# Kernel optimization log

Hardware: AMD Instinct MI355X
Metric: run time of the kernel (lower is better)

The kernel has to match this reference:

```python
import jax, jax.numpy as jnp
import numpy as np

N = 20000          # nodes
E = 320000         # edges
H = 128            # hidden_channels
A = 512            # aerial feature dim
SPOT = 20000
DIST_UNIT = 50
NEMB = SPOT // DIST_UNIT
RATIO = 0.25       # neighbor_ratio


def setup_inputs() -> dict:
    key = jax.random.key(0)
    ks = jax.random.split(key, 12)
    x = jax.random.normal(ks[0], (N, H), jnp.float32)
    edge_index = jax.random.randint(ks[1], (2, E), 0, N)
    distances = jax.random.randint(ks[2], (E,), 0, SPOT)
    aerial_emb = jax.random.normal(ks[3], (N, A), jnp.float32)
    s = lambda k, shape, fan: jax.random.normal(k, shape, jnp.float32) / np.sqrt(fan).astype(np.float32)
    W_lin = s(ks[4], (H, H), H)
    b_lin = jnp.zeros((H,), jnp.float32)
    W_q = s(ks[5], (H + A + H, H), H + A + H)
    b_q = jnp.zeros((H,), jnp.float32)
    W_v = s(ks[6], (H, H), H)
    b_v = jnp.zeros((H,), jnp.float32)
    dist_table = jax.random.normal(ks[7], (NEMB, H), jnp.float32)  # init.normal_ like torch
    W_l = s(ks[8], (H, H), H)   # SAGE lin_l (neighbor aggr), with bias
    b_l = jnp.zeros((H,), jnp.float32)
    W_r = s(ks[9], (H, H), H)   # SAGE lin_r (root), no bias in PyG default
    return dict(x=x, edge_index=edge_index, distances=distances, aerial_emb=aerial_emb,
                W_lin=W_lin, b_lin=b_lin, W_q=W_q, b_q=b_q, W_v=W_v, b_v=b_v,
                dist_table=dist_table, W_l=W_l, b_l=b_l, W_r=W_r)


def reference(x, edge_index, distances, aerial_emb, W_lin, b_lin, W_q, b_q, W_v, b_v, dist_table, W_l, b_l, W_r):
    n = x.shape[0]
    e = edge_index.shape[1]
    k = int(e * RATIO)  # static: number of sampled edges

    x = x @ W_lin + b_lin                                  # [N, H]
    src, tgt = edge_index[0], edge_index[1]
    source_x = x[src]                                      # [E, H]
    target_x = x[tgt]                                      # [E, H]
    source_aerial = aerial_emb[src]                        # [E, A]
    dist_x = dist_table[distances // DIST_UNIT]            # [E, H]

    query = jnp.concatenate([source_x, source_aerial, dist_x], axis=1) @ W_q + b_q  # [E, H]
    value = target_x @ W_v + b_v                           # [E, H]
    logits = -jnp.linalg.norm(query - value, axis=1)       # [E]
    logprob = jax.nn.log_softmax(logits, axis=0)

    # torch.multinomial(prob, k) without replacement == Gumbel top-k on log-probs
    u = jax.random.uniform(jax.random.key(42), (e,), jnp.float32)
    gumbel = -jnp.log(-jnp.log(u + 1e-20) + 1e-20)
    _, sel = jax.lax.top_k(logprob + gumbel, k)            # [k] selected edge ids
    src_s = src[sel]
    tgt_s = tgt[sel]

    # SAGEConv (mean aggregation): out = lin_l(mean_j x_j) + lin_r(x)
    msg = jax.ops.segment_sum(x[src_s], tgt_s, num_segments=n)              # [N, H]
    deg = jax.ops.segment_sum(jnp.ones((k,), x.dtype), tgt_s, num_segments=n)
    aggr = msg / jnp.maximum(deg, 1.0)[:, None]
    out = aggr @ W_l + b_l + x @ W_r                       # [N, H]
    return out
```

## Files before the change

### kernel.cpp

```cpp
#include <hip/hip_runtime.h>
#include <stdint.h>

#define N_NODES 20000
#define E_EDGES 320000
#define H_DIM 128
#define A_DIM 512
#define NEMB_N 400
#define K_SEL 80000u
#define NB1 16384
#define NB2 16384
#define CAND_MAX 8192
#define LO_F (-128.0f)
#define SCALE1 (16384.0f / 160.0f)

struct SelState {
    int b1; unsigned cum1; unsigned r1;
    int b2; unsigned cum2; unsigned r2;
    unsigned long long T;
};

__device__ __forceinline__ uint32_t rotl32(uint32_t x, int r) {
    return (x << r) | (x >> (32 - r));
}

__device__ __forceinline__ void threefry2x32(uint32_t k0, uint32_t k1,
                                             uint32_t& x0, uint32_t& x1) {
    uint32_t ks0 = k0, ks1 = k1, ks2 = k0 ^ k1 ^ 0x1BD11BDAu;
    x0 += ks0; x1 += ks1;
    x0 += x1; x1 = rotl32(x1, 13); x1 ^= x0;
    x0 += x1; x1 = rotl32(x1, 15); x1 ^= x0;
    x0 += x1; x1 = rotl32(x1, 26); x1 ^= x0;
    x0 += x1; x1 = rotl32(x1, 6);  x1 ^= x0;
    x0 += ks1; x1 += ks2 + 1u;
    x0 += x1; x1 = rotl32(x1, 17); x1 ^= x0;
    x0 += x1; x1 = rotl32(x1, 29); x1 ^= x0;
    x0 += x1; x1 = rotl32(x1, 16); x1 ^= x0;
    x0 += x1; x1 = rotl32(x1, 24); x1 ^= x0;
    x0 += ks2; x1 += ks0 + 2u;
    x0 += x1; x1 = rotl32(x1, 13); x1 ^= x0;
    x0 += x1; x1 = rotl32(x1, 15); x1 ^= x0;
    x0 += x1; x1 = rotl32(x1, 26); x1 ^= x0;
    x0 += x1; x1 = rotl32(x1, 6);  x1 ^= x0;
    x0 += ks0; x1 += ks1 + 3u;
    x0 += x1; x1 = rotl32(x1, 17); x1 ^= x0;
    x0 += x1; x1 = rotl32(x1, 29); x1 ^= x0;
    x0 += x1; x1 = rotl32(x1, 16); x1 ^= x0;
    x0 += x1; x1 = rotl32(x1, 24); x1 ^= x0;
    x0 += ks1; x1 += ks2 + 4u;
    x0 += x1; x1 = rotl32(x1, 13); x1 ^= x0;
    x0 += x1; x1 = rotl32(x1, 15); x1 ^= x0;
    x0 += x1; x1 = rotl32(x1, 26); x1 ^= x0;
    x0 += x1; x1 = rotl32(x1, 6);  x1 ^= x0;
    x0 += ks2; x1 += ks0 + 5u;
}

__global__ __launch_bounds__(256) void k_rand(float* __restrict__ u) {
    int e = blockIdx.x * 256 + threadIdx.x;
    if (e >= E_EDGES) return;
    uint32_t x0 = 0u, x1 = (uint32_t)e;
    threefry2x32(0u, 42u, x0, x1);
    uint32_t bits = x0 ^ x1;
    uint32_t fb = (bits >> 9) | 0x3f800000u;
    u[e] = __uint_as_float(fb) - 1.0f;
}

__global__ __launch_bounds__(128) void k_node(
    const float* __restrict__ x, const float* __restrict__ aerial,
    const float* __restrict__ Wlin, const float* __restrict__ blin,
    const float* __restrict__ Wq, const float* __restrict__ bq,
    const float* __restrict__ Wv, const float* __restrict__ bv,
    float* __restrict__ xl32, float* __restrict__ q32, float* __restrict__ v32) {
    __shared__ float xinT[H_DIM][8];
    __shared__ float xsT[H_DIM][8];
    __shared__ float aerT[A_DIM][8];
    const int j = threadIdx.x;
    const int n0 = blockIdx.x * 8;
#pragma unroll
    for (int m = 0; m < 8; ++m) xinT[j][m] = x[(size_t)(n0 + m) * H_DIM + j];
#pragma unroll
    for (int m = 0; m < 8; ++m)
#pragma unroll
        for (int c = 0; c < 4; ++c)
            aerT[c * H_DIM + j][m] = aerial[(size_t)(n0 + m) * A_DIM + c * H_DIM + j];
    __syncthreads();
    float acc[8];
    {
        float bj = blin[j];
#pragma unroll
        for (int m = 0; m < 8; ++m) acc[m] = bj;
        for (int k = 0; k < H_DIM; ++k) {
            float w = Wlin[k * H_DIM + j];
            const float4* xp = (const float4*)&xinT[k][0];
            float4 a0 = xp[0], a1 = xp[1];
            acc[0] = fmaf(a0.x, w, acc[0]); acc[1] = fmaf(a0.y, w, acc[1]);
            acc[2] = fmaf(a0.z, w, acc[2]); acc[3] = fmaf(a0.w, w, acc[3]);
            acc[4] = fmaf(a1.x, w, acc[4]); acc[5] = fmaf(a1.y, w, acc[5]);
            acc[6] = fmaf(a1.z, w, acc[6]); acc[7] = fmaf(a1.w, w, acc[7]);
        }
    }
#pragma unroll
    for (int m = 0; m < 8; ++m) {
        xsT[j][m] = acc[m];
        xl32[(size_t)(n0 + m) * H_DIM + j] = acc[m];
    }
    __syncthreads();
    {
        float bj = bv[j];
        float av[8];
#pragma unroll
        for (int m = 0; m < 8; ++m) av[m] = bj;
        for (int k = 0; k < H_DIM; ++k) {
            float w = Wv[k * H_DIM + j];
            const float4* xp = (const float4*)&xsT[k][0];
            float4 a0 = xp[0], a1 = xp[1];
            av[0] = fmaf(a0.x, w, av[0]); av[1] = fmaf(a0.y, w, av[1]);
            av[2] = fmaf(a0.z, w, av[2]); av[3] = fmaf(a0.w, w, av[3]);
            av[4] = fmaf(a1.x, w, av[4]); av[5] = fmaf(a1.y, w, av[5]);
            av[6] = fmaf(a1.z, w, av[6]); av[7] = fmaf(a1.w, w, av[7]);
        }
#pragma unroll
        for (int m = 0; m < 8; ++m) v32[(size_t)(n0 + m) * H_DIM + j] = av[m];
    }
    {
        float bj = bq[j];
        float aq[8];
#pragma unroll
        for (int m = 0; m < 8; ++m) aq[m] = bj;
        for (int k = 0; k < H_DIM; ++k) {
            float w = Wq[k * H_DIM + j];
            const float4* xp = (const float4*)&xsT[k][0];
            float4 a0 = xp[0], a1 = xp[1];
            aq[0] = fmaf(a0.x, w, aq[0]); aq[1] = fmaf(a0.y, w, aq[1]);
            aq[2] = fmaf(a0.z, w, aq[2]); aq[3] = fmaf(a0.w, w, aq[3]);
            aq[4] = fmaf(a1.x, w, aq[4]); aq[5] = fmaf(a1.y, w, aq[5]);
            aq[6] = fmaf(a1.z, w, aq[6]); aq[7] = fmaf(a1.w, w, aq[7]);
        }
        for (int k = 0; k < A_DIM; ++k) {
            float w = Wq[(size_t)(H_DIM + k) * H_DIM + j];
            const float4* xp = (const float4*)&aerT[k][0];
            float4 a0 = xp[0], a1 = xp[1];
            aq[0] = fmaf(a0.x, w, aq[0]); aq[1] = fmaf(a0.y, w, aq[1]);
            aq[2] = fmaf(a0.z, w, aq[2]); aq[3] = fmaf(a0.w, w, aq[3]);
            aq[4] = fmaf(a1.x, w, aq[4]); aq[5] = fmaf(a1.y, w, aq[5]);
            aq[6] = fmaf(a1.z, w, aq[6]); aq[7] = fmaf(a1.w, w, aq[7]);
        }
#pragma unroll
        for (int m = 0; m < 8; ++m) q32[(size_t)(n0 + m) * H_DIM + j] = aq[m];
    }
}

__global__ __launch_bounds__(128) void k_dist(
    const float* __restrict__ dtab, const float* __restrict__ Wq,
    float* __restrict__ dq32) {
    __shared__ float dsT[H_DIM][8];
    const int j = threadIdx.x;
    const int n0 = blockIdx.x * 8;
#pragma unroll
    for (int m = 0; m < 8; ++m) dsT[j][m] = dtab[(size_t)(n0 + m) * H_DIM + j];
    __syncthreads();
    float acc[8];
#pragma unroll
    for (int m = 0; m < 8; ++m) acc[m] = 0.0f;
    for (int k = 0; k < H_DIM; ++k) {
        float w = Wq[(size_t)(H_DIM + A_DIM + k) * H_DIM + j];
        const float4* xp = (const float4*)&dsT[k][0];
        float4 a0 = xp[0], a1 = xp[1];
        acc[0] = fmaf(a0.x, w, acc[0]); acc[1] = fmaf(a0.y, w, acc[1]);
        acc[2] = fmaf(a0.z, w, acc[2]); acc[3] = fmaf(a0.w, w, acc[3]);
        acc[4] = fmaf(a1.x, w, acc[4]); acc[5] = fmaf(a1.y, w, acc[5]);
        acc[6] = fmaf(a1.z, w, acc[6]); acc[7] = fmaf(a1.w, w, acc[7]);
    }
#pragma unroll
    for (int m = 0; m < 8; ++m) dq32[(size_t)(n0 + m) * H_DIM + j] = acc[m];
}

__global__ __launch_bounds__(256) void k_score(
    const int* __restrict__ ei, const int* __restrict__ dist,
    const float* __restrict__ q32, const float* __restrict__ v32,
    const float* __restrict__ dq32, const float* __restrict__ u,
    unsigned long long* __restrict__ keys, float* __restrict__ s32o) {
    const int half = threadIdx.x >> 5, lane = threadIdx.x & 31;
    const int e = blockIdx.x * 8 + half;
    const int s = ei[e], t = ei[E_EDGES + e];
    const int db = dist[e] / 50;
    const float4* qp = (const float4*)(q32 + (size_t)s * H_DIM);
    const float4* vp = (const float4*)(v32 + (size_t)t * H_DIM);
    const float4* dp = (const float4*)(dq32 + (size_t)db * H_DIM);
    float4 q = qp[lane], v = vp[lane], d = dp[lane];
    float dx = q.x + d.x - v.x;
    float dy = q.y + d.y - v.y;
    float dz = q.z + d.z - v.z;
    float dw = q.w + d.w - v.w;
    float ss = fmaf(dx, dx, fmaf(dy, dy, fmaf(dz, dz, dw * dw)));
#pragma unroll
    for (int o = 16; o > 0; o >>= 1) ss += __shfl_xor(ss, o, 64);
    if (lane == 0) {
        float nrm = sqrtf(ss);
        float uu = u[e];
        float a = -logf(uu + 1e-20f);
        float g = -logf(a + 1e-20f);
        float score = g - nrm;
        int ib = __float_as_int(score);
        unsigned m32 = (ib < 0) ? ~(unsigned)ib : ((unsigned)ib | 0x80000000u);
        keys[e] = ((unsigned long long)m32 << 32) | (unsigned)(0xFFFFFFFFu - (unsigned)e);
        s32o[e] = score;
    }
}

__device__ __forceinline__ int bin1_of(float s) {
    float t = (s - LO_F) * SCALE1;
    int b = (int)t;
    return min(max(b, 0), NB1 - 1);
}
__device__ __forceinline__ int bin2_of(float s, int b1) {
    float t = (s - LO_F) * SCALE1;
    float frac = t - (float)b1;
    int b = (int)(frac * (float)NB2);
    return min(max(b, 0), NB2 - 1);
}

__global__ __launch_bounds__(256) void k_hist1(const float* __restrict__ s32,
                                               unsigned* __restrict__ hist1) {
    int e = blockIdx.x * 256 + threadIdx.x;
    if (e >= E_EDGES) return;
    atomicAdd(&hist1[bin1_of(s32[e])], 1u);
}

__global__ __launch_bounds__(256) void k_hist2(const float* __restrict__ s32,
                                               const SelState* __restrict__ st,
                                               unsigned* __restrict__ hist2) {
    int e = blockIdx.x * 256 + threadIdx.x;
    if (e >= E_EDGES) return;
    float s = s32[e];
    int b1 = bin1_of(s);
    if (b1 != st->b1) return;
    atomicAdd(&hist2[bin2_of(s, b1)], 1u);
}

__global__ __launch_bounds__(256) void k_scan(const unsigned* __restrict__ hist,
                                              SelState* st, int phase) {
    __shared__ unsigned csum[256];
    __shared__ unsigned bins[64];
    __shared__ int selc;
    __shared__ unsigned cumbase;
    const int t = threadIdx.x;
    const unsigned target = (phase == 1) ? K_SEL : st->r1;
    unsigned s = 0;
    for (int i = 0; i < 64; ++i) s += hist[t * 64 + i];
    csum[t] = s;
    __syncthreads();
    if (t == 0) {
        unsigned cum = 0; int c = 255;
        for (; c >= 0; --c) {
            if (cum + csum[c] >= target) break;
            cum += csum[c];
        }
        selc = c; cumbase = cum;
    }
    __syncthreads();
    if (t < 64) bins[t] = hist[selc * 64 + t];
    __syncthreads();
    if (t == 0) {
        unsigned cum = cumbase; int b = -1;
        for (int i = 63; i >= 0; --i) {
            if (cum + bins[i] >= target) { b = selc * 64 + i; break; }
            cum += bins[i];
        }
        unsigned r = target - cum;
        if (phase == 1) { st->b1 = b; st->cum1 = cum; st->r1 = r; }
        else           { st->b2 = b; st->cum2 = cum; st->r2 = r; }
    }
}

__global__ __launch_bounds__(256) void k_collect(
    const float* __restrict__ s32, const unsigned long long* __restrict__ keys,
    const SelState* __restrict__ st, unsigned long long* __restrict__ cand,
    unsigned* __restrict__ cnt) {
    int e = blockIdx.x * 256 + threadIdx.x;
    if (e >= E_EDGES) return;
    float s = s32[e];
    int b1 = bin1_of(s);
    if (b1 != st->b1) return;
    if (bin2_of(s, b1) != st->b2) return;
    unsigned p = atomicAdd(cnt, 1u);
    if (p < CAND_MAX) cand[p] = keys[e];
}

__global__ __launch_bounds__(256) void k_thresh(
    const unsigned long long* __restrict__ cand, const unsigned* __restrict__ cnt,
    SelState* st) {
    int c = (int)min(*cnt, (unsigned)CAND_MAX);
    unsigned r2 = st->r2;
    for (int i = threadIdx.x; i < c; i += blockDim.x) {
        unsigned long long ki = cand[i];
        unsigned g = 0;
        for (int j = 0; j < c; ++j) g += (cand[j] > ki);
        if (g == r2 - 1) st->T = ki;
    }
}

__global__ __launch_bounds__(256) void k_scatter(
    const int* __restrict__ ei, const unsigned long long* __restrict__ keys,
    const SelState* __restrict__ st, const float* __restrict__ xl32,
    float* __restrict__ msg, float* __restrict__ deg) {
    const int wid = threadIdx.x >> 6, lane = threadIdx.x & 63;
    const int e = blockIdx.x * 4 + wid;
    if (keys[e] >= st->T) {
        int sidx = ei[e], tidx = ei[E_EDGES + e];
        const float* xp = xl32 + (size_t)sidx * H_DIM;
        float* mp = msg + (size_t)tidx * H_DIM;
        const int h = lane * 2;
        atomicAdd(&mp[h], xp[h]);
        atomicAdd(&mp[h + 1], xp[h + 1]);
        if (lane == 0) atomicAdd(&deg[tidx], 1.0f);
    }
}

__global__ __launch_bounds__(128) void k_out(
    const float* __restrict__ msg, const float* __restrict__ deg,
    const float* __restrict__ xl32, const float* __restrict__ Wl,
    const float* __restrict__ bl, const float* __restrict__ Wr,
    float* __restrict__ out) {
    __shared__ float axT[H_DIM][8];
    __shared__ float xxT[H_DIM][8];
    const int j = threadIdx.x;
    const int n0 = blockIdx.x * 8;
#pragma unroll
    for (int m = 0; m < 8; ++m) {
        float d = fmaxf(deg[n0 + m], 1.0f);
        axT[j][m] = msg[(size_t)(n0 + m) * H_DIM + j] / d;
        xxT[j][m] = xl32[(size_t)(n0 + m) * H_DIM + j];
    }
    __syncthreads();
    float acc[8];
    float bj = bl[j];
#pragma unroll
    for (int m = 0; m < 8; ++m) acc[m] = bj;
    for (int k = 0; k < H_DIM; ++k) {
        float wl = Wl[k * H_DIM + j];
        float wr = Wr[k * H_DIM + j];
        const float4* ap = (const float4*)&axT[k][0];
        const float4* xp = (const float4*)&xxT[k][0];
        float4 a0 = ap[0], a1 = ap[1];
        float4 x0 = xp[0], x1 = xp[1];
        acc[0] = fmaf(a0.x, wl, fmaf(x0.x, wr, acc[0]));
        acc[1] = fmaf(a0.y, wl, fmaf(x0.y, wr, acc[1]));
        acc[2] = fmaf(a0.z, wl, fmaf(x0.z, wr, acc[2]));
        acc[3] = fmaf(a0.w, wl, fmaf(x0.w, wr, acc[3]));
        acc[4] = fmaf(a1.x, wl, fmaf(x1.x, wr, acc[4]));
        acc[5] = fmaf(a1.y, wl, fmaf(x1.y, wr, acc[5]));
        acc[6] = fmaf(a1.z, wl, fmaf(x1.z, wr, acc[6]));
        acc[7] = fmaf(a1.w, wl, fmaf(x1.w, wr, acc[7]));
    }
#pragma unroll
    for (int m = 0; m < 8; ++m) out[(size_t)(n0 + m) * H_DIM + j] = acc[m];
}

extern "C" void kernel_launch(void* const* d_in, const int* in_sizes, int n_in,
                              void* d_out, int out_size, void* d_ws, size_t ws_size,
                              hipStream_t stream) {
    const float* x      = (const float*)d_in[0];
    const int*   ei     = (const int*)d_in[1];
    const int*   dist   = (const int*)d_in[2];
    const float* aerial = (const float*)d_in[3];
    const float* Wlin   = (const float*)d_in[4];
    const float* blin   = (const float*)d_in[5];
    const float* Wq     = (const float*)d_in[6];
    const float* bq     = (const float*)d_in[7];
    const float* Wv     = (const float*)d_in[8];
    const float* bv     = (const float*)d_in[9];
    const float* dtab   = (const float*)d_in[10];
    const float* Wl     = (const float*)d_in[11];
    const float* bl     = (const float*)d_in[12];
    const float* Wr     = (const float*)d_in[13];
    float* out = (float*)d_out;

    char* ws = (char*)d_ws;
    size_t off = 0;
    auto alloc = [&](size_t bytes) -> void* {
        void* p = ws + off;
        off += (bytes + 255) & ~(size_t)255;
        return p;
    };
    float* q32  = (float*)alloc((size_t)N_NODES * H_DIM * 4);
    float* v32  = (float*)alloc((size_t)N_NODES * H_DIM * 4);
    float* dq32 = (float*)alloc((size_t)NEMB_N * H_DIM * 4);
    unsigned long long* keys = (unsigned long long*)alloc((size_t)E_EDGES * 8);
    float* xl32 = (float*)alloc((size_t)N_NODES * H_DIM * 4);
    float* urnd = (float*)alloc((size_t)E_EDGES * 4);
    float* s32  = (float*)alloc((size_t)E_EDGES * 4);
    char* zbase = ws + off;
    float* msg  = (float*)alloc((size_t)N_NODES * H_DIM * 4);
    float* deg  = (float*)alloc((size_t)N_NODES * 4);
    unsigned* hist1 = (unsigned*)alloc((size_t)NB1 * 4);
    unsigned* hist2 = (unsigned*)alloc((size_t)NB2 * 4);
    unsigned long long* cand = (unsigned long long*)alloc((size_t)CAND_MAX * 8);
    unsigned* counters = (unsigned*)alloc(256);
    SelState* st = (SelState*)alloc(256);
    size_t zlen = (size_t)((ws + off) - zbase);

    hipMemsetAsync(zbase, 0, zlen, stream);

    k_node<<<N_NODES / 8, 128, 0, stream>>>(x, aerial, Wlin, blin, Wq, bq, Wv, bv,
                                            xl32, q32, v32);
    k_dist<<<NEMB_N / 8, 128, 0, stream>>>(dtab, Wq, dq32);
    k_rand<<<(E_EDGES + 255) / 256, 256, 0, stream>>>(urnd);
    k_score<<<E_EDGES / 8, 256, 0, stream>>>(ei, dist, q32, v32, dq32, urnd, keys, s32);
    k_hist1<<<(E_EDGES + 255) / 256, 256, 0, stream>>>(s32, hist1);
    k_scan<<<1, 256, 0, stream>>>(hist1, st, 1);
    k_hist2<<<(E_EDGES + 255) / 256, 256, 0, stream>>>(s32, st, hist2);
    k_scan<<<1, 256, 0, stream>>>(hist2, st, 2);
    k_collect<<<(E_EDGES + 255) / 256, 256, 0, stream>>>(s32, keys, st, cand, &counters[0]);
    k_thresh<<<1, 256, 0, stream>>>(cand, &counters[0], st);
    k_scatter<<<E_EDGES / 4, 256, 0, stream>>>(ei, keys, st, xl32, msg, deg);
    k_out<<<N_NODES / 8, 128, 0, stream>>>(msg, deg, xl32, Wl, bl, Wr, out);
}
```

Baseline: 487.8 us.

## Register-tile node GEMMs over 32 nodes and fuse RNG and histogram into scoring

The node projection kernel now handles 32 nodes per block, and each thread computes a 4x8 register tile, so every weight load is reused across 8 nodes and 4 columns. The Wv and Wq-x passes share one loop, and aerial features are streamed through shared memory in four chunks. The separate Threefry RNG kernel and first histogram kernel are folded into the scoring kernel, which removes two launches and the round trips through global memory for the random values and scores. In exchange, fewer blocks launch, register pressure is higher, and the scoring kernel now issues global atomics.

New measurement: 570.7 us. 17.0% more time.

```diff
diff --git a/kernel.cpp b/kernel.cpp
--- a/kernel.cpp
+++ b/kernel.cpp
@@ -12,6 +12,7 @@
 #define CAND_MAX 8192
 #define LO_F (-128.0f)
 #define SCALE1 (16384.0f / 160.0f)
+#define KN_M 32
 
 struct SelState {
     int b1; unsigned cum1; unsigned r1;
@@ -54,98 +55,134 @@
     x0 += ks2; x1 += ks0 + 5u;
 }
 
-__global__ __launch_bounds__(256) void k_rand(float* __restrict__ u) {
-    int e = blockIdx.x * 256 + threadIdx.x;
-    if (e >= E_EDGES) return;
-    uint32_t x0 = 0u, x1 = (uint32_t)e;
-    threefry2x32(0u, 42u, x0, x1);
-    uint32_t bits = x0 ^ x1;
-    uint32_t fb = (bits >> 9) | 0x3f800000u;
-    u[e] = __uint_as_float(fb) - 1.0f;
-}
-
 __global__ __launch_bounds__(128) void k_node(
     const float* __restrict__ x, const float* __restrict__ aerial,
     const float* __restrict__ Wlin, const float* __restrict__ blin,
     const float* __restrict__ Wq, const float* __restrict__ bq,
     const float* __restrict__ Wv, const float* __restrict__ bv,
     float* __restrict__ xl32, float* __restrict__ q32, float* __restrict__ v32) {
-    __shared__ float xinT[H_DIM][8];
-    __shared__ float xsT[H_DIM][8];
-    __shared__ float aerT[A_DIM][8];
-    const int j = threadIdx.x;
-    const int n0 = blockIdx.x * 8;
-#pragma unroll
-    for (int m = 0; m < 8; ++m) xinT[j][m] = x[(size_t)(n0 + m) * H_DIM + j];
-#pragma unroll
-    for (int m = 0; m < 8; ++m)
-#pragma unroll
-        for (int c = 0; c < 4; ++c)
-            aerT[c * H_DIM + j][m] = aerial[(size_t)(n0 + m) * A_DIM + c * H_DIM + j];
-    __syncthreads();
-    float acc[8];
+    __shared__ float bufA[H_DIM][KN_M + 4];
+    __shared__ float bufX[H_DIM][KN_M + 4];
+    const int tid = threadIdx.x;
+    const int mg = tid >> 5;
+    const int jj = tid & 31;
+    const int nb = mg * 8;
+    const int n0 = blockIdx.x * KN_M;
+    const int c0 = jj, c1 = jj + 32, c2 = jj + 64, c3 = jj + 96;
+
+    for (int m = 0; m < KN_M; ++m)
+        bufA[tid][m] = x[(size_t)(n0 + m) * H_DIM + tid];
+    __syncthreads();
+
+    float accL[4][8];
     {
-        float bj = blin[j];
-#pragma unroll
-        for (int m = 0; m < 8; ++m) acc[m] = bj;
+        float b0 = blin[c0], b1 = blin[c1], b2 = blin[c2], b3 = blin[c3];
+#pragma unroll
+        for (int i = 0; i < 8; ++i) {
+            accL[0][i] = b0; accL[1][i] = b1; accL[2][i] = b2; accL[3][i] = b3;
+        }
+    }
+#pragma unroll 4
+    for (int k = 0; k < H_DIM; ++k) {
+        const float4 xa = *(const float4*)&bufA[k][nb];
+        const float4 xb = *(const float4*)&bufA[k][nb + 4];
+        const float w0 = Wlin[k * H_DIM + c0];
+        const float w1 = Wlin[k * H_DIM + c1];
+        const float w2 = Wlin[k * H_DIM + c2];
+        const float w3 = Wlin[k * H_DIM + c3];
+        const float xv[8] = {xa.x, xa.y, xa.z, xa.w, xb.x, xb.y, xb.z, xb.w};
+#pragma unroll
+        for (int i = 0; i < 8; ++i) {
+            accL[0][i] = fmaf(xv[i], w0, accL[0][i]);
+            accL[1][i] = fmaf(xv[i], w1, accL[1][i]);
+            accL[2][i] = fmaf(xv[i], w2, accL[2][i]);
+            accL[3][i] = fmaf(xv[i], w3, accL[3][i]);
+        }
+    }
+#pragma unroll
+    for (int c = 0; c < 4; ++c) {
+        const int col = jj + c * 32;
+#pragma unroll
+        for (int i = 0; i < 8; ++i) {
+            xl32[(size_t)(n0 + nb + i) * H_DIM + col] = accL[c][i];
+            bufX[col][nb + i] = accL[c][i];
+        }
+    }
+    __syncthreads();
+
+    float accV[4][8], accQ[4][8];
+    {
+        float v0 = bv[c0], v1 = bv[c1], v2 = bv[c2], v3 = bv[c3];
+        float q0 = bq[c0], q1 = bq[c1], q2 = bq[c2], q3 = bq[c3];
+#pragma unroll
+        for (int i = 0; i < 8; ++i) {
+            accV[0][i] = v0; accV[1][i] = v1; accV[2][i] = v2; accV[3][i] = v3;
+            accQ[0][i] = q0; accQ[1][i] = q1; accQ[2][i] = q2; accQ[3][i] = q3;
+        }
+    }
+#pragma unroll 2
+    for (int k = 0; k < H_DIM; ++k) {
+        const float4 xa = *(const float4*)&bufX[k][nb];
+        const float4 xb = *(const float4*)&bufX[k][nb + 4];
+        const float wv0 = Wv[k * H_DIM + c0];
+        const float wv1 = Wv[k * H_DIM + c1];
+        const float wv2 = Wv[k * H_DIM + c2];
+        const float wv3 = Wv[k * H_DIM + c3];
+        const float wq0 = Wq[k * H_DIM + c0];
+        const float wq1 = Wq[k * H_DIM + c1];
+        const float wq2 = Wq[k * H_DIM + c2];
+        const float wq3 = Wq[k * H_DIM + c3];
+        const float xv[8] = {xa.x, xa.y, xa.z, xa.w, xb.x, xb.y, xb.z, xb.w};
+#pragma unroll
+        for (int i = 0; i < 8; ++i) {
+            accV[0][i] = fmaf(xv[i], wv0, accV[0][i]);
+            accV[1][i] = fmaf(xv[i], wv1, accV[1][i]);
+            accV[2][i] = fmaf(xv[i], wv2, accV[2][i]);
+            accV[3][i] = fmaf(xv[i], wv3, accV[3][i]);
+            accQ[0][i] = fmaf(xv[i], wq0, accQ[0][i]);
+            accQ[1][i] = fmaf(xv[i], wq1, accQ[1][i]);
+            accQ[2][i] = fmaf(xv[i], wq2, accQ[2][i]);
+            accQ[3][i] = fmaf(xv[i], wq3, accQ[3][i]);
+        }
+    }
+#pragma unroll
+    for (int c = 0; c < 4; ++c) {
+        const int col = jj + c * 32;
+#pragma unroll
+        for (int i = 0; i < 8; ++i)
+            v32[(size_t)(n0 + nb + i) * H_DIM + col] = accV[c][i];
+    }
+
+    for (int ch = 0; ch < 4; ++ch) {
+        __syncthreads();
+        for (int m = 0; m < KN_M; ++m)
+            bufA[tid][m] = aerial[(size_t)(n0 + m) * A_DIM + ch * H_DIM + tid];
+        __syncthreads();
+        const float* Wqc = Wq + (size_t)(H_DIM + ch * H_DIM) * H_DIM;
+#pragma unroll 4
         for (int k = 0; k < H_DIM; ++k) {
-            float w = Wlin[k * H_DIM + j];
-            const float4* xp = (const float4*)&xinT[k][0];
-            float4 a0 = xp[0], a1 = xp[1];
-            acc[0] = fmaf(a0.x, w, acc[0]); acc[1] = fmaf(a0.y, w, acc[1]);
-            acc[2] = fmaf(a0.z, w, acc[2]); acc[3] = fmaf(a0.w, w, acc[3]);
-            acc[4] = fmaf(a1.x, w, acc[4]); acc[5] = fmaf(a1.y, w, acc[5]);
-            acc[6] = fmaf(a1.z, w, acc[6]); acc[7] = fmaf(a1.w, w, acc[7]);
-        }
-    }
-#pragma unroll
-    for (int m = 0; m < 8; ++m) {
-        xsT[j][m] = acc[m];
-        xl32[(size_t)(n0 + m) * H_DIM + j] = acc[m];
-    }
-    __syncthreads();
-    {
-        float bj = bv[j];
-        float av[8];
-#pragma unroll
-        for (int m = 0; m < 8; ++m) av[m] = bj;
-        for (int k = 0; k < H_DIM; ++k) {
-            float w = Wv[k * H_DIM + j];
-            const float4* xp = (const float4*)&xsT[k][0];
-            float4 a0 = xp[0], a1 = xp[1];
-            av[0] = fmaf(a0.x, w, av[0]); av[1] = fmaf(a0.y, w, av[1]);
-            av[2] = fmaf(a0.z, w, av[2]); av[3] = fmaf(a0.w, w, av[3]);
-            av[4] = fmaf(a1.x, w, av[4]); av[5] = fmaf(a1.y, w, av[5]);
-            av[6] = fmaf(a1.z, w, av[6]); av[7] = fmaf(a1.w, w, av[7]);
-        }
-#pragma unroll
-        for (int m = 0; m < 8; ++m) v32[(size_t)(n0 + m) * H_DIM + j] = av[m];
-    }
-    {
-        float bj = bq[j];
-        float aq[8];
-#pragma unroll
-        for (int m = 0; m < 8; ++m) aq[m] = bj;
-        for (int k = 0; k < H_DIM; ++k) {
-            float w = Wq[k * H_DIM + j];
-            const float4* xp = (const float4*)&xsT[k][0];
-            float4 a0 = xp[0], a1 = xp[1];
-            aq[0] = fmaf(a0.x, w, aq[0]); aq[1] = fmaf(a0.y, w, aq[1]);
-            aq[2] = fmaf(a0.z, w, aq[2]); aq[3] = fmaf(a0.w, w, aq[3]);
-            aq[4] = fmaf(a1.x, w, aq[4]); aq[5] = fmaf(a1.y, w, aq[5]);
-            aq[6] = fmaf(a1.z, w, aq[6]); aq[7] = fmaf(a1.w, w, aq[7]);
-        }
-        for (int k = 0; k < A_DIM; ++k) {
-            float w = Wq[(size_t)(H_DIM + k) * H_DIM + j];
-            const float4* xp = (const float4*)&aerT[k][0];
-            float4 a0 = xp[0], a1 = xp[1];
-            aq[0] = fmaf(a0.x, w, aq[0]); aq[1] = fmaf(a0.y, w, aq[1]);
-            aq[2] = fmaf(a0.z, w, aq[2]); aq[3] = fmaf(a0.w, w, aq[3]);
-            aq[4] = fmaf(a1.x, w, aq[4]); aq[5] = fmaf(a1.y, w, aq[5]);
-            aq[6] = fmaf(a1.z, w, aq[6]); aq[7] = fmaf(a1.w, w, aq[7]);
-        }
-#pragma unroll
-        for (int m = 0; m < 8; ++m) q32[(size_t)(n0 + m) * H_DIM + j] = aq[m];
+            const float4 xa = *(const float4*)&bufA[k][nb];
+            const float4 xb = *(const float4*)&bufA[k][nb + 4];
+            const float w0 = Wqc[k * H_DIM + c0];
+            const float w1 = Wqc[k * H_DIM + c1];
+            const float w2 = Wqc[k * H_DIM + c2];
+            const float w3 = Wqc[k * H_DIM + c3];
+            const float xv[8] = {xa.x, xa.y, xa.z, xa.w, xb.x, xb.y, xb.z, xb.w};
+#pragma unroll
+            for (int i = 0; i < 8; ++i) {
+                accQ[0][i] = fmaf(xv[i], w0, accQ[0][i]);
+                accQ[1][i] = fmaf(xv[i], w1, accQ[1][i]);
+                accQ[2][i] = fmaf(xv[i], w2, accQ[2][i]);
+                accQ[3][i] = fmaf(xv[i], w3, accQ[3][i]);
+            }
+        }
+    }
+#pragma unroll
+    for (int c = 0; c < 4; ++c) {
+        const int col = jj + c * 32;
+#pragma unroll
+        for (int i = 0; i < 8; ++i)
+            q32[(size_t)(n0 + nb + i) * H_DIM + col] = accQ[c][i];
     }
 }
 
@@ -174,11 +211,24 @@
     for (int m = 0; m < 8; ++m) dq32[(size_t)(n0 + m) * H_DIM + j] = acc[m];
 }
 
+__device__ __forceinline__ int bin1_of(float s) {
+    float t = (s - LO_F) * SCALE1;
+    int b = (int)t;
+    return min(max(b, 0), NB1 - 1);
+}
+__device__ __forceinline__ int bin2_of(float s, int b1) {
+    float t = (s - LO_F) * SCALE1;
+    float frac = t - (float)b1;
+    int b = (int)(frac * (float)NB2);
+    return min(max(b, 0), NB2 - 1);
+}
+
 __global__ __launch_bounds__(256) void k_score(
     const int* __restrict__ ei, const int* __restrict__ dist,
     const float* __restrict__ q32, const float* __restrict__ v32,
-    const float* __restrict__ dq32, const float* __restrict__ u,
-    unsigned long long* __restrict__ keys, float* __restrict__ s32o) {
+    const float* __restrict__ dq32,
+    unsigned long long* __restrict__ keys, float* __restrict__ s32o,
+    unsigned* __restrict__ hist1) {
     const int half = threadIdx.x >> 5, lane = threadIdx.x & 31;
     const int e = blockIdx.x * 8 + half;
     const int s = ei[e], t = ei[E_EDGES + e];
@@ -194,9 +244,12 @@
     float ss = fmaf(dx, dx, fmaf(dy, dy, fmaf(dz, dz, dw * dw)));
 #pragma unroll
     for (int o = 16; o > 0; o >>= 1) ss += __shfl_xor(ss, o, 64);
+    uint32_t r0 = 0u, r1 = (uint32_t)e;
+    threefry2x32(0u, 42u, r0, r1);
+    uint32_t fb = ((r0 ^ r1) >> 9) | 0x3f800000u;
+    float uu = __uint_as_float(fb) - 1.0f;
     if (lane == 0) {
         float nrm = sqrtf(ss);
-        float uu = u[e];
         float a = -logf(uu + 1e-20f);
         float g = -logf(a + 1e-20f);
         float score = g - nrm;
@@ -204,26 +257,8 @@
         unsigned m32 = (ib < 0) ? ~(unsigned)ib : ((unsigned)ib | 0x80000000u);
         keys[e] = ((unsigned long long)m32 << 32) | (unsigned)(0xFFFFFFFFu - (unsigned)e);
         s32o[e] = score;
-    }
-}
-
-__device__ __forceinline__ int bin1_of(float s) {
-    float t = (s - LO_F) * SCALE1;
-    int b = (int)t;
-    return min(max(b, 0), NB1 - 1);
-}
-__device__ __forceinline__ int bin2_of(float s, int b1) {
-    float t = (s - LO_F) * SCALE1;
-    float frac = t - (float)b1;
-    int b = (int)(frac * (float)NB2);
-    return min(max(b, 0), NB2 - 1);
-}
-
-__global__ __launch_bounds__(256) void k_hist1(const float* __restrict__ s32,
-                                               unsigned* __restrict__ hist1) {
-    int e = blockIdx.x * 256 + threadIdx.x;
-    if (e >= E_EDGES) return;
-    atomicAdd(&hist1[bin1_of(s32[e])], 1u);
+        atomicAdd(&hist1[bin1_of(score)], 1u);
+    }
 }
 
 __global__ __launch_bounds__(256) void k_hist2(const float* __restrict__ s32,
@@ -387,7 +422,6 @@
     float* dq32 = (float*)alloc((size_t)NEMB_N * H_DIM * 4);
     unsigned long long* keys = (unsigned long long*)alloc((size_t)E_EDGES * 8);
     float* xl32 = (float*)alloc((size_t)N_NODES * H_DIM * 4);
-    float* urnd = (float*)alloc((size_t)E_EDGES * 4);
     float* s32  = (float*)alloc((size_t)E_EDGES * 4);
     char* zbase = ws + off;
     float* msg  = (float*)alloc((size_t)N_NODES * H_DIM * 4);
@@ -401,12 +435,10 @@
 
     hipMemsetAsync(zbase, 0, zlen, stream);
 
-    k_node<<<N_NODES / 8, 128, 0, stream>>>(x, aerial, Wlin, blin, Wq, bq, Wv, bv,
-                                            xl32, q32, v32);
+    k_node<<<N_NODES / KN_M, 128, 0, stream>>>(x, aerial, Wlin, blin, Wq, bq, Wv, bv,
+                                               xl32, q32, v32);
     k_dist<<<NEMB_N / 8, 128, 0, stream>>>(dtab, Wq, dq32);
-    k_rand<<<(E_EDGES + 255) / 256, 256, 0, stream>>>(urnd);
-    k_score<<<E_EDGES / 8, 256, 0, stream>>>(ei, dist, q32, v32, dq32, urnd, keys, s32);
-    k_hist1<<<(E_EDGES + 255) / 256, 256, 0, stream>>>(s32, hist1);
+    k_score<<<E_EDGES / 8, 256, 0, stream>>>(ei, dist, q32, v32, dq32, keys, s32, hist1);
     k_scan<<<1, 256, 0, stream>>>(hist1, st, 1);
     k_hist2<<<(E_EDGES + 255) / 256, 256, 0, stream>>>(s32, st, hist2);
     k_scan<<<1, 256, 0, stream>>>(hist2, st, 2);
```
